# Kernel tuning notes

Measured on AMD Instinct MI355X. Metric: run time of the kernel, lower is better.

## Reference

```python
import jax, jax.numpy as jnp
import numpy as np

H = W = 128          # feature-map height/width
WS = 8               # window size
SHIFT = 4            # cyclic shift (ws // 2)
HEADS = 3
C = 96               # hidden size (head_dim = 32)
MLP_FACTOR = 4
N = WS * WS          # tokens per window
NW = (H // WS) * (W // WS)  # windows per image


def _rel_pos_index():
    coords = np.stack(np.meshgrid(np.arange(WS), np.arange(WS), indexing='ij')).reshape(2, -1)
    rel = (coords[:, :, None] - coords[:, None, :]).transpose(1, 2, 0)
    rel[:, :, 0] += WS - 1
    rel[:, :, 1] += WS - 1
    rel[:, :, 0] *= 2 * WS - 1
    return rel.sum(-1)  # (N, N) int


def _window_partition_np(img):  # (H, W) -> (NW, N)
    x = img.reshape(H // WS, WS, W // WS, WS)
    return x.transpose(0, 2, 1, 3).reshape(-1, N)


def _attn_mask():
    img = np.zeros((H, W))
    cnt = 0
    sl = (slice(0, -WS), slice(-WS, -SHIFT), slice(-SHIFT, None))
    for hs in sl:
        for ws_ in sl:
            img[hs, ws_] = cnt
            cnt += 1
    win = _window_partition_np(img)
    return np.where(win[:, None, :] != win[:, :, None], -100.0, 0.0).astype(np.float32)


REL_IDX = jnp.asarray(_rel_pos_index().reshape(-1))   # (N*N,)
ATTN_MASK = jnp.asarray(_attn_mask())                 # (NW, N, N)


def _layernorm(x, g, b, eps=1e-5):
    m = x.mean(-1, keepdims=True)
    v = ((x - m) ** 2).mean(-1, keepdims=True)
    return (x - m) * jax.lax.rsqrt(v + eps) * g + b


def setup_inputs() -> dict:
    key = jax.random.key(0)
    ks = jax.random.split(key, 8)
    B = 16
    s = 0.02  # random_normal_initializer(0.0, 0.02)
    return {
        'x': jax.random.normal(ks[0], (B, H * W, C), jnp.float32),
        'ln1_g': jnp.ones((C,), jnp.float32),
        'ln1_b': jnp.zeros((C,), jnp.float32),
        'qkv_w': jax.random.normal(ks[1], (C, 3 * C), jnp.float32) * s,
        'qkv_b': jnp.zeros((3 * C,), jnp.float32),
        'proj_w': jax.random.normal(ks[2], (C, C), jnp.float32) * s,
        'bias_table': jax.random.normal(ks[3], ((2 * WS - 1) ** 2, HEADS), jnp.float32) * s,
        'ln2_g': jnp.ones((C,), jnp.float32),
        'ln2_b': jnp.zeros((C,), jnp.float32),
        'mlp_w1': jax.random.normal(ks[4], (C, MLP_FACTOR * C), jnp.float32) * s,
        'mlp_w2': jax.random.normal(ks[5], (MLP_FACTOR * C, C), jnp.float32) * s,
    }


def reference(x, ln1_g, ln1_b, qkv_w, qkv_b, proj_w, bias_table, ln2_g, ln2_b, mlp_w1, mlp_w2):
    B = x.shape[0]
    shortcut = x
    h = _layernorm(x, ln1_g, ln1_b).reshape(B, H, W, C)
    # cyclic shift
    h = jnp.roll(h, (-SHIFT, -SHIFT), axis=(1, 2))
    # window partition: (B*NW, N, C)
    h = h.reshape(B, H // WS, WS, W // WS, WS, C).transpose(0, 1, 3, 2, 4, 5).reshape(B * NW, N, C)
    # windowed MHSA
    qkv = h @ qkv_w + qkv_b
    qkv = qkv.reshape(B * NW, N, 3, HEADS, C // HEADS).transpose(2, 0, 3, 1, 4)
    q, k, v = qkv[0], qkv[1], qkv[2]
    scale = (C // HEADS) ** -0.5
    attn = jnp.einsum('whnd,whmd->whnm', q * scale, k)
    bias = bias_table[REL_IDX].reshape(N, N, HEADS).transpose(2, 0, 1)
    attn = attn + bias[None]
    attn = attn.reshape(B, NW, HEADS, N, N) + ATTN_MASK[None, :, None]
    attn = jax.nn.softmax(attn, axis=-1).reshape(B * NW, HEADS, N, N)
    out = jnp.einsum('whnm,whmd->whnd', attn, v).transpose(0, 2, 1, 3).reshape(B * NW, N, C)
    out = out @ proj_w
    # window reverse + un-shift
    out = out.reshape(B, H // WS, W // WS, WS, WS, C).transpose(0, 1, 3, 2, 4, 5).reshape(B, H, W, C)
    out = jnp.roll(out, (SHIFT, SHIFT), axis=(1, 2)).reshape(B, H * W, C)
    x = shortcut + out
    # MLP branch
    h2 = _layernorm(x, ln2_g, ln2_b)
    h2 = jax.nn.gelu(h2 @ mlp_w1) @ mlp_w2
    return x + h2
```

## Files before the change

### kernel.cpp

```cpp
#include <hip/hip_runtime.h>

#define SHIFT 4

typedef __bf16 bf16x8 __attribute__((ext_vector_type(8)));
typedef __bf16 bf16x4 __attribute__((ext_vector_type(4)));
typedef float  f32x4  __attribute__((ext_vector_type(4)));

#define WS_W1T  36864
#define WS_W2C  73728
#define WS_BIAS_BYTES 221184

__global__ __launch_bounds__(256)
void swin_prep_kernel(const float* __restrict__ qkvw, const float* __restrict__ projw,
                      const float* __restrict__ w1, const float* __restrict__ w2,
                      const float* __restrict__ btab,
                      __bf16* __restrict__ ws)
{
  const int i = blockIdx.x * 256 + threadIdx.x;
  if (i < 36864) {
    const int fi = i >> 9, e = i & 511;
    const int lane = e >> 3, j = e & 7;
    const int l15 = lane & 15;
    const int kk  = (lane >> 4) * 8 + j;
    float v;
    if (fi < 54) {
      const int c = fi / 18, rem = fi % 18, t = rem / 3, ks = rem % 3;
      v = qkvw[(ks * 32 + kk) * 288 + c * 96 + t * 16 + l15];
    } else {
      const int f2 = fi - 54, t = f2 / 3, ks = f2 % 3;
      v = projw[(ks * 32 + kk) * 96 + t * 16 + l15];
    }
    ws[i] = (__bf16)v;
  } else if (i < 73728) {
    const int j = i - WS_W1T;
    const int col = j / 96, kk = j - col * 96;
    ws[i] = (__bf16)w1[kk * 384 + col];
  } else if (i < 110592) {
    const int j = i - WS_W2C;
    const int cc = j / 6144, r2 = j - cc * 6144;
    const int o = r2 / 64, jl = r2 - o * 64;
    ws[i] = (__bf16)w2[(cc * 64 + jl) * 96 + o];
  } else {
    const int jj = i - 110592;
    const int h = jj >> 12, n = (jj >> 6) & 63, m = jj & 63;
    const int dy = (n >> 3) - (m >> 3), dx = (n & 7) - (m & 7);
    float* biasf = (float*)((char*)ws + WS_BIAS_BYTES);
    biasf[jj] = btab[((dy + 7) * 15 + (dx + 7)) * 3 + h];
  }
}

#define LDA 104
#define LDV 72

__global__ __launch_bounds__(256, 4)
void swin_attn_kernel(const float* __restrict__ x,
                      const float* __restrict__ ln1g, const float* __restrict__ ln1b,
                      const __bf16* __restrict__ ws, const float* __restrict__ qkvb,
                      float* __restrict__ out)
{
  __shared__ __align__(16) char lds[40448];
  __bf16* h_s = (__bf16*)lds;
  __bf16* k_s = (__bf16*)(lds + 13312);
  __bf16* v_s = (__bf16*)(lds + 26624);

  const float* biasf = (const float*)((const char*)ws + WS_BIAS_BYTES);

  const int tid  = threadIdx.x;
  const int lane = tid & 63;
  const int wv   = tid >> 6;
  const int l15  = lane & 15;
  const int g4   = lane >> 4;
  const int blk  = blockIdx.x;
  const int b    = blk >> 8;
  const int wy   = (blk >> 4) & 15;
  const int wx   = blk & 15;

  {
    const int t = tid >> 2, p = tid & 3;
    const int ti = t >> 3, tj = t & 7;
    const int iy = (wy * 8 + ti + SHIFT) & 127;
    const int ix = (wx * 8 + tj + SHIFT) & 127;
    const float* rowp = x + ((size_t)(b * 16384 + iy * 128 + ix)) * 96 + p * 24;
    float vb[24];
    float s = 0.f, ss = 0.f;
#pragma unroll
    for (int u = 0; u < 6; ++u) {
      f32x4 f = *(const f32x4*)(rowp + 4 * u);
#pragma unroll
      for (int e = 0; e < 4; ++e) { float q = f[e]; vb[4*u+e] = q; s += q; ss += q*q; }
    }
    s  += __shfl_xor(s, 1);  s  += __shfl_xor(s, 2);
    ss += __shfl_xor(ss, 1); ss += __shfl_xor(ss, 2);
    const float mean = s * (1.f / 96.f);
    const float var  = ss * (1.f / 96.f) - mean * mean;
    const float rstd = rsqrtf(var + 1e-5f);
#pragma unroll
    for (int u = 0; u < 6; ++u) {
      f32x4 gg = *(const f32x4*)(ln1g + p * 24 + 4 * u);
      f32x4 bb = *(const f32x4*)(ln1b + p * 24 + 4 * u);
      f32x4 nv;
#pragma unroll
      for (int e = 0; e < 4; ++e) nv[e] = (vb[4*u+e] - mean) * rstd * gg[e] + bb[e];
      *(bf16x4*)&h_s[t * LDA + p * 24 + 4 * u] = __builtin_convertvector(nv, bf16x4);
    }
  }

  const float qscale = 0.17677669529663687f;
  const __bf16* fbase = ws + (size_t)lane * 8;
  const int rowb = 16 * wv;
  bf16x8 aq3[3];
#pragma unroll
  for (int c = 0; c < 3; ++c) {
    bf16x8 wf[6][3];
#pragma unroll
    for (int t = 0; t < 6; ++t)
#pragma unroll
      for (int ks = 0; ks < 3; ++ks)
        wf[t][ks] = *(const bf16x8*)(fbase + (size_t)(c * 18 + t * 3 + ks) * 512);
    f32x4 acc[6];
#pragma unroll
    for (int t = 0; t < 6; ++t) {
      const float bv = qkvb[c * 96 + t * 16 + l15];
      f32x4 a4 = {bv, bv, bv, bv};
      acc[t] = a4;
    }
#pragma unroll
    for (int ks = 0; ks < 3; ++ks) {
      bf16x8 a = *(const bf16x8*)&h_s[(rowb + l15) * LDA + ks * 32 + 8 * g4];
#pragma unroll
      for (int t = 0; t < 6; ++t)
        acc[t] = __builtin_amdgcn_mfma_f32_16x16x32_bf16(a, wf[t][ks], acc[t], 0, 0, 0);
    }
    if (c == 0) {
#pragma unroll
      for (int t = 0; t < 6; ++t) {
        const int col = (t >> 1) * 32 + (t & 1) * 16 + l15;
#pragma unroll
        for (int r = 0; r < 4; ++r)
          k_s[(rowb + 4 * g4 + r) * LDA + col] = (__bf16)(acc[t][r] * qscale);
      }
#pragma unroll
      for (int h = 0; h < 3; ++h)
        aq3[h] = *(const bf16x8*)&k_s[(rowb + l15) * LDA + h * 32 + 8 * g4];
    } else if (c == 1) {
#pragma unroll
      for (int t = 0; t < 6; ++t) {
        const int col = (t >> 1) * 32 + (t & 1) * 16 + l15;
#pragma unroll
        for (int r = 0; r < 4; ++r)
          k_s[(rowb + 4 * g4 + r) * LDA + col] = (__bf16)acc[t][r];
      }
    } else {
#pragma unroll
      for (int t = 0; t < 6; ++t) {
        const int head = t >> 1, dim = (t & 1) * 16 + l15;
        *(bf16x4*)&v_s[(head * 32 + dim) * LDV + rowb + 4 * g4] =
            __builtin_convertvector(acc[t], bf16x4);
      }
    }
  }

  __syncthreads();

  int qry[4], qrx[4];
#pragma unroll
  for (int r = 0; r < 4; ++r) {
    const int row = rowb + 4 * g4 + r;
    const int ti2 = row >> 3, tj2 = row & 7;
    qry[r] = (wy == 15) ? (ti2 < 4 ? 1 : 2) : 0;
    qrx[r] = (wx == 15) ? (tj2 < 4 ? 1 : 2) : 0;
  }
  const f32x4 zf = {0.f, 0.f, 0.f, 0.f};
  f32x4 ovA[3][2];
#pragma unroll
  for (int h = 0; h < 3; ++h) {
    const float* bh = biasf + h * 4096;
    float bv[4][4];
#pragma unroll
    for (int n = 0; n < 4; ++n)
#pragma unroll
      for (int r = 0; r < 4; ++r)
        bv[n][r] = bh[(rowb + 4 * g4 + r) * 64 + n * 16 + l15];

    f32x4 sc[4];
#pragma unroll
    for (int n = 0; n < 4; ++n) {
      bf16x8 bk = *(const bf16x8*)&k_s[(n * 16 + l15) * LDA + h * 32 + 8 * g4];
      sc[n] = __builtin_amdgcn_mfma_f32_16x16x32_bf16(aq3[h], bk, zf, 0, 0, 0);
    }
#pragma unroll
    for (int n = 0; n < 4; ++n) {
      const int colt = n * 16 + l15;
      const int ki = colt >> 3, kj = colt & 7;
      const int kry = (wy == 15) ? (ki < 4 ? 1 : 2) : 0;
      const int krx = (wx == 15) ? (kj < 4 ? 1 : 2) : 0;
#pragma unroll
      for (int r = 0; r < 4; ++r) {
        const float mk = (qry[r] == kry && qrx[r] == krx) ? 0.f : -100.f;
        sc[n][r] += bv[n][r] + mk;
      }
    }
    float mx[4], sm[4];
#pragma unroll
    for (int r = 0; r < 4; ++r) {
      float m = fmaxf(fmaxf(sc[0][r], sc[1][r]), fmaxf(sc[2][r], sc[3][r]));
      m = fmaxf(m, __shfl_xor(m, 1)); m = fmaxf(m, __shfl_xor(m, 2));
      m = fmaxf(m, __shfl_xor(m, 4)); m = fmaxf(m, __shfl_xor(m, 8));
      mx[r] = m; sm[r] = 0.f;
    }
#pragma unroll
    for (int n = 0; n < 4; ++n)
#pragma unroll
      for (int r = 0; r < 4; ++r) {
        float p = __expf(sc[n][r] - mx[r]); sc[n][r] = p; sm[r] += p;
      }
#pragma unroll
    for (int r = 0; r < 4; ++r) {
      float s2 = sm[r];
      s2 += __shfl_xor(s2, 1); s2 += __shfl_xor(s2, 2);
      s2 += __shfl_xor(s2, 4); s2 += __shfl_xor(s2, 8);
      sm[r] = __builtin_amdgcn_rcpf(s2);
    }
#pragma unroll
    for (int n = 0; n < 4; ++n)
#pragma unroll
      for (int r = 0; r < 4; ++r)
        h_s[(rowb + 4 * g4 + r) * LDA + n * 16 + l15] = (__bf16)sc[n][r];
    f32x4 ov[2] = {zf, zf};
#pragma unroll
    for (int ks = 0; ks < 2; ++ks) {
      bf16x8 pa = *(const bf16x8*)&h_s[(rowb + l15) * LDA + ks * 32 + 8 * g4];
#pragma unroll
      for (int t2 = 0; t2 < 2; ++t2) {
        bf16x8 vb2 = *(const bf16x8*)&v_s[(h * 32 + t2 * 16 + l15) * LDV + ks * 32 + 8 * g4];
        ov[t2] = __builtin_amdgcn_mfma_f32_16x16x32_bf16(pa, vb2, ov[t2], 0, 0, 0);
      }
    }
#pragma unroll
    for (int t2 = 0; t2 < 2; ++t2)
#pragma unroll
      for (int r = 0; r < 4; ++r)
        ovA[h][t2][r] = ov[t2][r] * sm[r];
  }
#pragma unroll
  for (int h = 0; h < 3; ++h)
#pragma unroll
    for (int t2 = 0; t2 < 2; ++t2)
#pragma unroll
      for (int r = 0; r < 4; ++r)
        h_s[(rowb + 4 * g4 + r) * LDA + h * 32 + t2 * 16 + l15] = (__bf16)ovA[h][t2][r];

  f32x4 po[6];
#pragma unroll
  for (int t = 0; t < 6; ++t) po[t] = zf;
#pragma unroll
  for (int ks = 0; ks < 3; ++ks) {
    bf16x8 a = *(const bf16x8*)&h_s[(rowb + l15) * LDA + ks * 32 + 8 * g4];
#pragma unroll
    for (int t = 0; t < 6; ++t) {
      bf16x8 bb = *(const bf16x8*)(fbase + (size_t)(54 + t * 3 + ks) * 512);
      po[t] = __builtin_amdgcn_mfma_f32_16x16x32_bf16(a, bb, po[t], 0, 0, 0);
    }
  }
#pragma unroll
  for (int r = 0; r < 4; ++r) {
    const int row = rowb + 4 * g4 + r;
    const int ti2 = row >> 3, tj2 = row & 7;
    const int iy = (wy * 8 + ti2 + SHIFT) & 127;
    const int ix = (wx * 8 + tj2 + SHIFT) & 127;
    const size_t gbase = ((size_t)(b * 16384 + iy * 128 + ix)) * 96;
#pragma unroll
    for (int t = 0; t < 6; ++t) {
      const size_t gi = gbase + t * 16 + l15;
      out[gi] = x[gi] + po[t][r];
    }
  }
}

#define LDH 104
#define LDU 72
#define LDW1 104
#define LDW2 72

__global__ __launch_bounds__(256, 4)
void swin_mlp_kernel(const float* __restrict__ ln2g, const float* __restrict__ ln2b,
                     const __bf16* __restrict__ ws, float* xm)
{
  __shared__ __align__(16) char mlds[36352];
  __bf16* h_s = (__bf16*)mlds;
  __bf16* u_s = (__bf16*)(mlds + 13312);
  __bf16* w_s = (__bf16*)(mlds + 22528);

  const int tid = threadIdx.x, lane = tid & 63, wv = tid >> 6;
  const int l15 = lane & 15, g4 = lane >> 4;
  const size_t rowg = (size_t)blockIdx.x * 64;

  {
    const int t = tid >> 2, p = tid & 3;
    const float* rowp = xm + (rowg + t) * 96 + p * 24;
    float vb[24];
    float s = 0.f, ss = 0.f;
#pragma unroll
    for (int u = 0; u < 6; ++u) {
      f32x4 f = *(const f32x4*)(rowp + 4 * u);
#pragma unroll
      for (int e = 0; e < 4; ++e) { float q = f[e]; vb[4*u+e] = q; s += q; ss += q*q; }
    }
    s  += __shfl_xor(s, 1);  s  += __shfl_xor(s, 2);
    ss += __shfl_xor(ss, 1); ss += __shfl_xor(ss, 2);
    const float mean = s * (1.f / 96.f);
    const float var  = ss * (1.f / 96.f) - mean * mean;
    const float rstd = rsqrtf(var + 1e-5f);
#pragma unroll
    for (int u = 0; u < 6; ++u) {
      f32x4 gg = *(const f32x4*)(ln2g + p * 24 + 4 * u);
      f32x4 bb = *(const f32x4*)(ln2b + p * 24 + 4 * u);
      f32x4 nv;
#pragma unroll
      for (int e = 0; e < 4; ++e) nv[e] = (vb[4*u+e] - mean) * rstd * gg[e] + bb[e];
      *(bf16x4*)&h_s[t * LDH + p * 24 + 4 * u] = __builtin_convertvector(nv, bf16x4);
    }
  }
  __syncthreads();

  const int rowb = 16 * wv;
  const f32x4 zf = {0.f, 0.f, 0.f, 0.f};
  f32x4 acc[6];
#pragma unroll
  for (int t = 0; t < 6; ++t) acc[t] = zf;

  for (int cc = 0; cc < 6; ++cc) {
    {
      const __bf16* wsrc = ws + WS_W1T + cc * 6144;
#pragma unroll
      for (int m = tid; m < 768; m += 256) {
        const int row = m / 12, q4 = m - row * 12;
        *(uint4*)&w_s[row * LDW1 + q4 * 8] = *(const uint4*)&wsrc[row * 96 + q4 * 8];
      }
    }
    __syncthreads();
    f32x4 ua[4];
#pragma unroll
    for (int t = 0; t < 4; ++t) ua[t] = zf;
#pragma unroll
    for (int ks = 0; ks < 3; ++ks) {
      bf16x8 a = *(const bf16x8*)&h_s[(rowb + l15) * LDH + ks * 32 + 8 * g4];
#pragma unroll
      for (int t = 0; t < 4; ++t) {
        bf16x8 bb = *(const bf16x8*)&w_s[(t * 16 + l15) * LDW1 + ks * 32 + 8 * g4];
        ua[t] = __builtin_amdgcn_mfma_f32_16x16x32_bf16(a, bb, ua[t], 0, 0, 0);
      }
    }
#pragma unroll
    for (int t = 0; t < 4; ++t)
#pragma unroll
      for (int r = 0; r < 4; ++r) {
        const float v = ua[t][r];
        const float e = __expf(1.5957691216057308f * (v + 0.044715f * v * v * v));
        const float g = v - v * __builtin_amdgcn_rcpf(e + 1.f);
        u_s[(rowb + 4 * g4 + r) * LDU + t * 16 + l15] = (__bf16)g;
      }
    __syncthreads();
    {
      const __bf16* wsrc = ws + WS_W2C + cc * 6144;
#pragma unroll
      for (int m = tid; m < 768; m += 256) {
        const int row = m >> 3, q4 = m & 7;
        *(uint4*)&w_s[row * LDW2 + q4 * 8] = *(const uint4*)&wsrc[row * 64 + q4 * 8];
      }
    }
    __syncthreads();
#pragma unroll
    for (int ks = 0; ks < 2; ++ks) {
      bf16x8 pa = *(const bf16x8*)&u_s[(rowb + l15) * LDU + ks * 32 + 8 * g4];
#pragma unroll
      for (int t = 0; t < 6; ++t) {
        bf16x8 bb = *(const bf16x8*)&w_s[(t * 16 + l15) * LDW2 + ks * 32 + 8 * g4];
        acc[t] = __builtin_amdgcn_mfma_f32_16x16x32_bf16(pa, bb, acc[t], 0, 0, 0);
      }
    }
    __syncthreads();
  }
#pragma unroll
  for (int r = 0; r < 4; ++r) {
    const size_t gr = (rowg + rowb + 4 * g4 + r) * 96;
#pragma unroll
    for (int t = 0; t < 6; ++t) {
      const size_t gi = gr + t * 16 + l15;
      xm[gi] = xm[gi] + acc[t][r];
    }
  }
}

extern "C" void kernel_launch(void* const* d_in, const int* in_sizes, int n_in,
                              void* d_out, int out_size, void* d_ws, size_t ws_size,
                              hipStream_t stream) {
  (void)in_sizes; (void)n_in; (void)out_size; (void)ws_size;
  const float* x     = (const float*)d_in[0];
  const float* ln1g  = (const float*)d_in[1];
  const float* ln1b  = (const float*)d_in[2];
  const float* qkvw  = (const float*)d_in[3];
  const float* qkvb  = (const float*)d_in[4];
  const float* projw = (const float*)d_in[5];
  const float* btab  = (const float*)d_in[6];
  const float* ln2g  = (const float*)d_in[7];
  const float* ln2b  = (const float*)d_in[8];
  const float* w1    = (const float*)d_in[9];
  const float* w2    = (const float*)d_in[10];
  float* out = (float*)d_out;
  __bf16* ws = (__bf16*)d_ws;

  swin_prep_kernel<<<480, 256, 0, stream>>>(qkvw, projw, w1, w2, btab, ws);
  swin_attn_kernel<<<4096, 256, 0, stream>>>(x, ln1g, ln1b, ws, qkvb, out);
  swin_mlp_kernel<<<4096, 256, 0, stream>>>(ln2g, ln2b, ws, out);
}
```

Baseline: 189.4 us.

## Fuse attention and MLP kernels into a single per-window block kernel

Merges the attention kernel and the MLP kernel into one kernel that processes a shifted window end to end. The residual x+attn result stays in registers, LayerNorm2 is computed from them with cross-lane shuffles, and the MLP runs on the same rows. Only the final output is written. This removes the intermediate global write and read of the full activation tensor and one kernel launch. In exchange it raises register pressure, which could hurt occupancy, and it reuses LDS regions across phases.

New measurement: 166.6 us. -12.0%, faster.

```diff
diff --git a/kernel.cpp b/kernel.cpp
--- a/kernel.cpp
+++ b/kernel.cpp
@@ -5,6 +5,12 @@
 typedef __bf16 bf16x8 __attribute__((ext_vector_type(8)));
 typedef __bf16 bf16x4 __attribute__((ext_vector_type(4)));
 typedef float  f32x4  __attribute__((ext_vector_type(4)));
+
+#define LDA 104
+#define LDV 72
+#define LDU 72
+#define LDW1 104
+#define LDW2 72
 
 #define WS_W1T  36864
 #define WS_W2C  73728
@@ -49,19 +55,19 @@
   }
 }
 
-#define LDA 104
-#define LDV 72
-
 __global__ __launch_bounds__(256, 4)
-void swin_attn_kernel(const float* __restrict__ x,
-                      const float* __restrict__ ln1g, const float* __restrict__ ln1b,
-                      const __bf16* __restrict__ ws, const float* __restrict__ qkvb,
-                      float* __restrict__ out)
+void swin_block_kernel(const float* __restrict__ x,
+                       const float* __restrict__ ln1g, const float* __restrict__ ln1b,
+                       const __bf16* __restrict__ ws, const float* __restrict__ qkvb,
+                       const float* __restrict__ ln2g, const float* __restrict__ ln2b,
+                       float* __restrict__ out)
 {
   __shared__ __align__(16) char lds[40448];
   __bf16* h_s = (__bf16*)lds;
   __bf16* k_s = (__bf16*)(lds + 13312);
   __bf16* v_s = (__bf16*)(lds + 26624);
+  __bf16* u_s = (__bf16*)(lds + 13312);
+  __bf16* w_s = (__bf16*)(lds + 26624);
 
   const float* biasf = (const float*)((const char*)ws + WS_BIAS_BYTES);
 
@@ -262,69 +268,46 @@
       po[t] = __builtin_amdgcn_mfma_f32_16x16x32_bf16(a, bb, po[t], 0, 0, 0);
     }
   }
+
+  size_t gbase[4];
+  float xm[6][4];
 #pragma unroll
   for (int r = 0; r < 4; ++r) {
     const int row = rowb + 4 * g4 + r;
     const int ti2 = row >> 3, tj2 = row & 7;
     const int iy = (wy * 8 + ti2 + SHIFT) & 127;
     const int ix = (wx * 8 + tj2 + SHIFT) & 127;
-    const size_t gbase = ((size_t)(b * 16384 + iy * 128 + ix)) * 96;
-#pragma unroll
-    for (int t = 0; t < 6; ++t) {
-      const size_t gi = gbase + t * 16 + l15;
-      out[gi] = x[gi] + po[t][r];
-    }
-  }
-}
-
-#define LDH 104
-#define LDU 72
-#define LDW1 104
-#define LDW2 72
-
-__global__ __launch_bounds__(256, 4)
-void swin_mlp_kernel(const float* __restrict__ ln2g, const float* __restrict__ ln2b,
-                     const __bf16* __restrict__ ws, float* xm)
-{
-  __shared__ __align__(16) char mlds[36352];
-  __bf16* h_s = (__bf16*)mlds;
-  __bf16* u_s = (__bf16*)(mlds + 13312);
-  __bf16* w_s = (__bf16*)(mlds + 22528);
-
-  const int tid = threadIdx.x, lane = tid & 63, wv = tid >> 6;
-  const int l15 = lane & 15, g4 = lane >> 4;
-  const size_t rowg = (size_t)blockIdx.x * 64;
-
+    gbase[r] = ((size_t)(b * 16384 + iy * 128 + ix)) * 96;
+#pragma unroll
+    for (int t = 0; t < 6; ++t)
+      xm[t][r] = x[gbase[r] + t * 16 + l15] + po[t][r];
+  }
   {
-    const int t = tid >> 2, p = tid & 3;
-    const float* rowp = xm + (rowg + t) * 96 + p * 24;
-    float vb[24];
-    float s = 0.f, ss = 0.f;
-#pragma unroll
-    for (int u = 0; u < 6; ++u) {
-      f32x4 f = *(const f32x4*)(rowp + 4 * u);
-#pragma unroll
-      for (int e = 0; e < 4; ++e) { float q = f[e]; vb[4*u+e] = q; s += q; ss += q*q; }
-    }
-    s  += __shfl_xor(s, 1);  s  += __shfl_xor(s, 2);
-    ss += __shfl_xor(ss, 1); ss += __shfl_xor(ss, 2);
-    const float mean = s * (1.f / 96.f);
-    const float var  = ss * (1.f / 96.f) - mean * mean;
-    const float rstd = rsqrtf(var + 1e-5f);
-#pragma unroll
-    for (int u = 0; u < 6; ++u) {
-      f32x4 gg = *(const f32x4*)(ln2g + p * 24 + 4 * u);
-      f32x4 bb = *(const f32x4*)(ln2b + p * 24 + 4 * u);
-      f32x4 nv;
-#pragma unroll
-      for (int e = 0; e < 4; ++e) nv[e] = (vb[4*u+e] - mean) * rstd * gg[e] + bb[e];
-      *(bf16x4*)&h_s[t * LDH + p * 24 + 4 * u] = __builtin_convertvector(nv, bf16x4);
-    }
-  }
+    float g6[6], b6[6];
+#pragma unroll
+    for (int t = 0; t < 6; ++t) { g6[t] = ln2g[t * 16 + l15]; b6[t] = ln2b[t * 16 + l15]; }
+#pragma unroll
+    for (int r = 0; r < 4; ++r) {
+      float s = 0.f, ss = 0.f;
+#pragma unroll
+      for (int t = 0; t < 6; ++t) { s += xm[t][r]; ss += xm[t][r] * xm[t][r]; }
+      s  += __shfl_xor(s, 1);  s  += __shfl_xor(s, 2);
+      s  += __shfl_xor(s, 4);  s  += __shfl_xor(s, 8);
+      ss += __shfl_xor(ss, 1); ss += __shfl_xor(ss, 2);
+      ss += __shfl_xor(ss, 4); ss += __shfl_xor(ss, 8);
+      const float mean = s * (1.f / 96.f);
+      const float var  = ss * (1.f / 96.f) - mean * mean;
+      const float rstd = rsqrtf(var + 1e-5f);
+#pragma unroll
+      for (int t = 0; t < 6; ++t) {
+        const float h2 = (xm[t][r] - mean) * rstd * g6[t] + b6[t];
+        h_s[(rowb + 4 * g4 + r) * LDA + t * 16 + l15] = (__bf16)h2;
+      }
+    }
+  }
+
   __syncthreads();
 
-  const int rowb = 16 * wv;
-  const f32x4 zf = {0.f, 0.f, 0.f, 0.f};
   f32x4 acc[6];
 #pragma unroll
   for (int t = 0; t < 6; ++t) acc[t] = zf;
@@ -344,7 +327,7 @@
     for (int t = 0; t < 4; ++t) ua[t] = zf;
 #pragma unroll
     for (int ks = 0; ks < 3; ++ks) {
-      bf16x8 a = *(const bf16x8*)&h_s[(rowb + l15) * LDH + ks * 32 + 8 * g4];
+      bf16x8 a = *(const bf16x8*)&h_s[(rowb + l15) * LDA + ks * 32 + 8 * g4];
 #pragma unroll
       for (int t = 0; t < 4; ++t) {
         bf16x8 bb = *(const bf16x8*)&w_s[(t * 16 + l15) * LDW1 + ks * 32 + 8 * g4];
@@ -381,15 +364,12 @@
     }
     __syncthreads();
   }
-#pragma unroll
-  for (int r = 0; r < 4; ++r) {
-    const size_t gr = (rowg + rowb + 4 * g4 + r) * 96;
-#pragma unroll
-    for (int t = 0; t < 6; ++t) {
-      const size_t gi = gr + t * 16 + l15;
-      xm[gi] = xm[gi] + acc[t][r];
-    }
-  }
+
+#pragma unroll
+  for (int r = 0; r < 4; ++r)
+#pragma unroll
+    for (int t = 0; t < 6; ++t)
+      out[gbase[r] + t * 16 + l15] = xm[t][r] + acc[t][r];
 }
 
 extern "C" void kernel_launch(void* const* d_in, const int* in_sizes, int n_in,
@@ -411,6 +391,5 @@
   __bf16* ws = (__bf16*)d_ws;
 
   swin_prep_kernel<<<480, 256, 0, stream>>>(qkvw, projw, w1, w2, btab, ws);
-  swin_attn_kernel<<<4096, 256, 0, stream>>>(x, ln1g, ln1b, ws, qkvb, out);
-  swin_mlp_kernel<<<4096, 256, 0, stream>>>(ln2g, ln2b, ws, out);
+  swin_block_kernel<<<4096, 256, 0, stream>>>(x, ln1g, ln1b, ws, qkvb, ln2g, ln2b, out);
 }
```
